# Kernel optimization log

Hardware: AMD Instinct MI355X
Metric: run time of the kernel (lower is better)

Reference implementation:

```python
import jax, jax.numpy as jnp
import numpy as np

B, S, D, H, T, R = 2, 2048, 768, 12, 64, 50
DH = D // H
EPS = 1e-12


def setup_inputs() -> dict:
    key = jax.random.key(0)
    ks = jax.random.split(key, 12)
    w = lambda k, shape: jax.random.normal(k, shape, jnp.float32) * 0.02
    inp = {
        "hidden_states": jax.random.normal(ks[0], (B, S, D), jnp.float32),
        "tag_emb": w(ks[1], (T, D)),
        "sa_wq": w(ks[2], (D, D)), "sa_bq": jnp.zeros((D,), jnp.float32),
        "sa_wk": w(ks[3], (D, D)), "sa_bk": jnp.zeros((D,), jnp.float32),
        "sa_wv": w(ks[4], (D, D)), "sa_bv": jnp.zeros((D,), jnp.float32),
        "sa_wo": w(ks[5], (D, D)), "sa_bo": jnp.zeros((D,), jnp.float32),
        "sa_ln_g": jnp.ones((D,), jnp.float32), "sa_ln_b": jnp.zeros((D,), jnp.float32),
        "ca_wq": w(ks[6], (D, D)), "ca_bq": jnp.zeros((D,), jnp.float32),
        "ca_wk": w(ks[7], (D, D)), "ca_bk": jnp.zeros((D,), jnp.float32),
        "ca_wv": w(ks[8], (D, D)), "ca_bv": jnp.zeros((D,), jnp.float32),
        "ca_wo": w(ks[9], (D, D)), "ca_bo": jnp.zeros((D,), jnp.float32),
        "ca_ln_g": jnp.ones((D,), jnp.float32), "ca_ln_b": jnp.zeros((D,), jnp.float32),
        "ff_w1": w(ks[10], (D, 3072)), "ff_b1": jnp.zeros((3072,), jnp.float32),
        "ff_w2": w(ks[11], (3072, D)), "ff_b2": jnp.zeros((D,), jnp.float32),
        "ff_ln_g": jnp.ones((D,), jnp.float32), "ff_ln_b": jnp.zeros((D,), jnp.float32),
    }
    return inp


def _layernorm(x, g, b):
    m = jnp.mean(x, axis=-1, keepdims=True)
    v = jnp.mean(jnp.square(x - m), axis=-1, keepdims=True)
    return (x - m) * jax.lax.rsqrt(v + EPS) * g + b


def _bert_attention(x, kv, mask, wq, bq, wk, bk, wv, bv, wo, bo, ln_g, ln_b):
    # BertSelfAttention: multi-head attn; mask (if any) is ADDED to scores (HF semantics).
    Bq, Sq = x.shape[0], x.shape[1]
    Sk = kv.shape[1]
    q = (x @ wq + bq).reshape(Bq, Sq, H, DH)
    k = (kv @ wk + bk).reshape(Bq, Sk, H, DH)
    v = (kv @ wv + bv).reshape(Bq, Sk, H, DH)
    scores = jnp.einsum("bqhd,bkhd->bhqk", q, k) / jnp.sqrt(jnp.float32(DH))
    if mask is not None:
        scores = scores + mask  # additive 0/1 band mask, as in the source
    probs = jax.nn.softmax(scores, axis=-1)
    ctx = jnp.einsum("bhqk,bkhd->bqhd", probs, v).reshape(Bq, Sq, D)
    # BertSelfOutput: dense + residual + LayerNorm
    return _layernorm(ctx @ wo + bo + x, ln_g, ln_b)


def reference(hidden_states, tag_emb,
              sa_wq, sa_bq, sa_wk, sa_bk, sa_wv, sa_bv, sa_wo, sa_bo, sa_ln_g, sa_ln_b,
              ca_wq, ca_bq, ca_wk, ca_bk, ca_wv, ca_bv, ca_wo, ca_bo, ca_ln_g, ca_ln_b,
              ff_w1, ff_b1, ff_w2, ff_b2, ff_ln_g, ff_ln_b):
    Sd = hidden_states.shape[1]
    # banded mask: tril(+R) * triu(-R) -> 1 inside window, 0 outside (added to scores)
    i = jnp.arange(Sd)
    band = (jnp.abs(i[:, None] - i[None, :]) <= R).astype(hidden_states.dtype)  # [S,S]
    attn_out = _bert_attention(hidden_states, hidden_states, band,
                               sa_wq, sa_bq, sa_wk, sa_bk, sa_wv, sa_bv,
                               sa_wo, sa_bo, sa_ln_g, sa_ln_b)
    tags = jnp.broadcast_to(tag_emb[None], (hidden_states.shape[0], T, D))
    attn_out = _bert_attention(attn_out, tags, None,
                               ca_wq, ca_bq, ca_wk, ca_bk, ca_wv, ca_bv,
                               ca_wo, ca_bo, ca_ln_g, ca_ln_b)
    # BertIntermediate + BertOutput (exact erf gelu as in HF)
    inter = jax.nn.gelu(attn_out @ ff_w1 + ff_b1, approximate=False)
    return _layernorm(inter @ ff_w2 + ff_b2 + attn_out, ff_ln_g, ff_ln_b)
```

## Files before the change

### kernel.cpp

```cpp
#include <hip/hip_runtime.h>
#include <cstdint>
#include <cstddef>


typedef __bf16 bf16;
typedef __bf16 bf16x8 __attribute__((ext_vector_type(8)));
typedef __bf16 bf16x4 __attribute__((ext_vector_type(4)));
typedef __bf16 bf16x2 __attribute__((ext_vector_type(2)));
typedef float  floatx4 __attribute__((ext_vector_type(4)));

__device__ __forceinline__ void glds16(const bf16* g, bf16* l) {
  __builtin_amdgcn_global_load_lds((const __attribute__((address_space(1))) void*)g,
                                   (__attribute__((address_space(3))) void*)l, 16, 0, 0);
}

__device__ __forceinline__ float fexp2(float x) {
  float r;
  asm("v_exp_f32 %0, %1" : "=v"(r) : "v"(x));
  return r;
}

__global__ __launch_bounds__(256) void k_prep_all(const float* __restrict__ sa_bq,
                                                  const float* __restrict__ sa_bk,
                                                  const float* __restrict__ sa_bv,
                                                  const float* __restrict__ ca_bk,
                                                  const float* __restrict__ ca_bv,
                                                  const float* __restrict__ tag,
                                                  const float* __restrict__ X,
                                                  float* __restrict__ bQKV,
                                                  float* __restrict__ bKV2,
                                                  bf16* __restrict__ tagp,
                                                  bf16* __restrict__ Xb) {
  int b = blockIdx.x, t = threadIdx.x;
  if (b < 9) {
    int i = b * 256 + t;
    int s = i / 768, j = i - s * 768;
    const float* p = s == 0 ? sa_bq : (s == 1 ? sa_bk : sa_bv);
    bQKV[i] = p[j];
  } else if (b < 15) {
    int i = (b - 9) * 256 + t;
    int s = i / 768, j = i - s * 768;
    bKV2[i] = s == 0 ? ca_bk[j] : ca_bv[j];
  } else if (b < 399) {
    int i = (b - 15) * 256 + t;
    if (i < 64 * 768) tagp[i] = (bf16)tag[i];
    else tagp[i] = (bf16)0.f;
  } else {
    int i = ((b - 399) * 256 + t) * 8;
    float4 a = *(const float4*)(X + i);
    float4 b4 = *(const float4*)(X + i + 4);
    bf16x8 o;
    o[0] = (bf16)a.x; o[1] = (bf16)a.y; o[2] = (bf16)a.z; o[3] = (bf16)a.w;
    o[4] = (bf16)b4.x; o[5] = (bf16)b4.y; o[6] = (bf16)b4.z; o[7] = (bf16)b4.w;
    *(bf16x8*)(Xb + i) = o;
  }
}

__device__ __forceinline__ void transpose_body(const float* __restrict__ W,
                                               bf16* __restrict__ Wt,
                                               int K, int N, int n0, int k0,
                                               bf16 (*tile)[72]) {
  int t = threadIdx.x;
  int r = t >> 2, cg = (t & 3) * 16;
  const float* src = W + (size_t)(k0 + r) * N + n0 + cg;
  float tmp[16];
  *(float4*)&tmp[0]  = *(const float4*)(src);
  *(float4*)&tmp[4]  = *(const float4*)(src + 4);
  *(float4*)&tmp[8]  = *(const float4*)(src + 8);
  *(float4*)&tmp[12] = *(const float4*)(src + 12);
#pragma unroll
  for (int i = 0; i < 16; ++i) tile[r][cg + i] = (bf16)tmp[i];
  __syncthreads();
  bf16* dst = Wt + (size_t)(n0 + r) * K + k0 + cg;
#pragma unroll
  for (int g = 0; g < 2; ++g) {
    bf16x8 pack;
#pragma unroll
    for (int i = 0; i < 8; ++i) pack[i] = tile[cg + g * 8 + i][r];
    *(bf16x8*)(dst + g * 8) = pack;
  }
}

__global__ __launch_bounds__(256) void k_transpose4(const float* __restrict__ W0,
                                                    const float* __restrict__ W1,
                                                    const float* __restrict__ W2w,
                                                    const float* __restrict__ W3,
                                                    bf16* __restrict__ Wt) {
  __shared__ bf16 tile[64][72];
  int z = blockIdx.z;
  const float* W = z == 0 ? W0 : (z == 1 ? W1 : (z == 2 ? W2w : W3));
  transpose_body(W, Wt + (size_t)z * 768 * 768, 768, 768,
                 blockIdx.x * 64, blockIdx.y * 64, tile);
}

__global__ __launch_bounds__(256) void k_transpose_ff(const float* __restrict__ ff_w1,
                                                      const float* __restrict__ ff_w2,
                                                      bf16* __restrict__ Wall,
                                                      bf16* __restrict__ W2) {
  __shared__ bf16 tile[64][72];
  if (blockIdx.z == 0)
    transpose_body(ff_w1, Wall, 768, 3072, blockIdx.x * 64, blockIdx.y * 64, tile);
  else
    transpose_body(ff_w2, W2, 3072, 768, blockIdx.y * 64, blockIdx.x * 64, tile);
}

template <int BM, int BN, int KS, bool CF32>
__device__ __forceinline__ void gemm_body(const bf16* __restrict__ Ab,
                                          const bf16* __restrict__ Bt,
                                          const float* __restrict__ bias,
                                          void* __restrict__ Co,
                                          int N, int K, int ld, int act,
                                          int m0, int n0,
                                          bf16* __restrict__ As,
                                          bf16* __restrict__ Bs) {
  constexpr int MT = BM / 32;
  constexpr int NT = BN / 32;
  constexpr int KSTEP = 32 * KS;
  int tid = threadIdx.x;
  int lane = tid & 63, wave = tid >> 6;
  int l16 = lane & 15, quad = lane >> 4;
  int wm = wave & 1, wn = wave >> 1;
  int arow = tid >> 2, acol = (tid & 3) * 8;
  int ldst = arow * 32 + acol;

  const bf16* Ap = Ab + (size_t)(m0 + arow) * ld + acol;
  const bf16* Bp = Bt + (size_t)(n0 + arow) * ld + acol;

  auto stage = [&](int k, int buf) {
    bf16* Asb = As + buf * (KS * BM * 32);
    bf16* Bsb = Bs + buf * (KS * BN * 32);
#pragma unroll
    for (int ks = 0; ks < KS; ++ks) {
      glds16(Bp + k + ks * 32, Bsb + ks * BN * 32 + ldst);
      if constexpr (BN == 128) glds16(Bp + (size_t)64 * ld + k + ks * 32, Bsb + ks * BN * 32 + ldst + 2048);
      glds16(Ap + k + ks * 32, Asb + ks * BM * 32 + ldst);
      if constexpr (BM == 128) glds16(Ap + (size_t)64 * ld + k + ks * 32, Asb + ks * BM * 32 + ldst + 2048);
    }
  };

  floatx4 acc[MT][NT];
#pragma unroll
  for (int i = 0; i < MT; ++i)
#pragma unroll
    for (int j = 0; j < NT; ++j) acc[i][j] = floatx4{0.f, 0.f, 0.f, 0.f};

  stage(0, 0);
  __syncthreads();

  int cur = 0;
  for (int k = 0; k < K; k += KSTEP) {
    if (k + KSTEP < K) stage(k + KSTEP, cur ^ 1);
    bf16* Asb = As + cur * (KS * BM * 32);
    bf16* Bsb = Bs + cur * (KS * BN * 32);
#pragma unroll
    for (int ks = 0; ks < KS; ++ks) {
      bf16x8 a_frag[MT], b_frag[NT];
#pragma unroll
      for (int mt = 0; mt < MT; ++mt)
        a_frag[mt] = *(const bf16x8*)(Asb + ks * BM * 32 + (wm * (BM / 2) + mt * 16 + l16) * 32 + quad * 8);
#pragma unroll
      for (int nt = 0; nt < NT; ++nt)
        b_frag[nt] = *(const bf16x8*)(Bsb + ks * BN * 32 + (wn * (BN / 2) + nt * 16 + l16) * 32 + quad * 8);
#pragma unroll
      for (int mt = 0; mt < MT; ++mt)
#pragma unroll
        for (int nt = 0; nt < NT; ++nt)
          acc[mt][nt] = __builtin_amdgcn_mfma_f32_16x16x32_bf16(a_frag[mt], b_frag[nt], acc[mt][nt], 0, 0, 0);
    }
    __syncthreads();
    cur ^= 1;
  }

#pragma unroll
  for (int nt = 0; nt < NT; ++nt) {
    int col = n0 + wn * (BN / 2) + nt * 16 + l16;
    float bv = bias ? bias[col] : 0.f;
#pragma unroll
    for (int mt = 0; mt < MT; ++mt) {
#pragma unroll
      for (int r = 0; r < 4; ++r) {
        int row = m0 + wm * (BM / 2) + mt * 16 + quad * 4 + r;
        float v = acc[mt][nt][r] + bv;
        if (act) v = 0.5f * v * (1.f + erff(v * 0.70710678118654752f));
        if constexpr (CF32) ((float*)Co)[(size_t)row * N + col] = v;
        else ((bf16*)Co)[(size_t)row * N + col] = (bf16)v;
      }
    }
  }
}

template <int BM, int BN, int KS, bool CF32>
__global__ __launch_bounds__(256) void k_gemm(const bf16* __restrict__ Ab,
                                              const bf16* __restrict__ Bt,
                                              const float* __restrict__ bias,
                                              void* __restrict__ Cv,
                                              void* __restrict__ Cv2,
                                              int N, int K, int ld, int act) {
  __shared__ bf16 As[2 * KS * BM * 32];
  __shared__ bf16 Bs[2 * KS * BN * 32];
  int z = blockIdx.z;
  gemm_body<BM, BN, KS, CF32>(Ab + z * K, Bt + z * K, z == 0 ? bias : nullptr,
                              z == 0 ? Cv : Cv2, N, K, ld, act,
                              blockIdx.x * BM, blockIdx.y * BN, As, Bs);
}

__global__ __launch_bounds__(256) void k_gemm_q2kv(const bf16* __restrict__ A0,
                                                   const bf16* __restrict__ B0,
                                                   const float* __restrict__ bias0,
                                                   bf16* __restrict__ C0,
                                                   const bf16* __restrict__ A1,
                                                   const bf16* __restrict__ B1,
                                                   const float* __restrict__ bias1,
                                                   bf16* __restrict__ C1) {
  __shared__ bf16 As[2 * 2 * 64 * 32];
  __shared__ bf16 Bs[2 * 2 * 64 * 32];
  if (blockIdx.z == 0) {
    gemm_body<64, 64, 2, false>(A0, B0, bias0, C0, 768, 768, 768, 0,
                                blockIdx.x * 64, blockIdx.y * 64, As, Bs);
  } else {
    if (blockIdx.y != 0 || blockIdx.x >= 48) return;
    gemm_body<64, 64, 2, false>(A1, B1, bias1, C1, 1536, 768, 768, 0,
                                (blockIdx.x & 1) * 64, (blockIdx.x >> 1) * 64, As, Bs);
  }
}

__global__ __launch_bounds__(256) void k_attn_mfma(const bf16* __restrict__ Q, int ldq,
                                                   const bf16* __restrict__ Kp,
                                                   const bf16* __restrict__ Vp, int ldkv,
                                                   bf16* __restrict__ O,
                                                   int S, int Skv,
                                                   long long kv_bstride, int bandR) {
  const int NH = 12;
  int qt = blockIdx.x, bh = blockIdx.y;
  int bb = bh / NH, h = bh % NH;
  const bf16* Qb = Q + (size_t)bb * S * ldq + h * 64;
  const bf16* Kb = Kp + (size_t)bb * kv_bstride + h * 64;
  const bf16* Vb = Vp + (size_t)bb * kv_bstride + h * 64;
  bf16* Ob = O + (size_t)bb * S * 768 + h * 64;

  __shared__ __align__(16) char smem[47104];
  float* Obuf = (float*)smem;
  float* l0_arr = (float*)(smem + 16896);

  int tid = threadIdx.x, wave = tid >> 6, lane = tid & 63;
  int quad = lane >> 4, l16 = lane & 15;
  int qh = wave & 1, kh = wave >> 1;
  bf16 (*Psw)[40] = (bf16(*)[40])(smem + 36864 + wave * 2560);

  const float C1 = 0.18033688f;
  const float C2 = 1.44269504f;

  int r = tid >> 2, cg = (tid & 3) * 16;
  int vk0 = 2 * (tid & 31);
  int vd0 = 8 * (tid >> 5);
  int vcol = (vk0 + 16 * (vd0 >> 4)) & 63;

  bf16x8 aq[2][2];
#pragma unroll
  for (int mt = 0; mt < 2; ++mt) {
    const bf16* qsrc = Qb + (size_t)(qt * 64 + qh * 32 + mt * 16 + l16) * ldq;
#pragma unroll
    for (int ks = 0; ks < 2; ++ks) {
      bf16x8 t = *(const bf16x8*)(qsrc + ks * 32 + quad * 8);
#pragma unroll
      for (int e = 0; e < 8; ++e) t[e] = (bf16)((float)t[e] * C1);
      aq[mt][ks] = t;
    }
  }

  bf16x8 ones;
#pragma unroll
  for (int e = 0; e < 8; ++e) ones[e] = (bf16)1.f;

  bf16x8 kr0, kr1, vr0, vr1;
  {
    const bf16* ksrc = Kb + (size_t)r * ldkv + cg;
    kr0 = *(const bf16x8*)ksrc;
    kr1 = *(const bf16x8*)(ksrc + 8);
    const bf16* vsrc = Vb + (size_t)vk0 * ldkv + vd0;
    vr0 = *(const bf16x8*)vsrc;
    vr1 = *(const bf16x8*)(vsrc + ldkv);
  }

  floatx4 accl[2];
  floatx4 acc[2][4];
#pragma unroll
  for (int mt = 0; mt < 2; ++mt) {
    accl[mt] = floatx4{0.f, 0.f, 0.f, 0.f};
#pragma unroll
    for (int j = 0; j < 4; ++j) acc[mt][j] = floatx4{0.f, 0.f, 0.f, 0.f};
  }

  int qi0 = qt * 64 + qh * 32 + quad * 4;

  for (int kc = 0; kc < Skv; kc += 64) {
    int cur = (kc >> 6) & 1;
    bf16 (*Ks)[72] = (bf16(*)[72])(smem + cur * 9216);
    bf16 (*Vt)[72] = (bf16(*)[72])(smem + 18432 + cur * 9216);
    *(bf16x8*)&Ks[r][cg] = kr0;
    *(bf16x8*)&Ks[r][cg + 8] = kr1;
#pragma unroll
    for (int e = 0; e < 8; ++e) {
      bf16x2 p; p[0] = vr0[e]; p[1] = vr1[e];
      *(bf16x2*)&Vt[vd0 + e][vcol] = p;
    }
    if (kc + 64 < Skv) {
      const bf16* ksrc = Kb + (size_t)(kc + 64 + r) * ldkv + cg;
      kr0 = *(const bf16x8*)ksrc;
      kr1 = *(const bf16x8*)(ksrc + 8);
      const bf16* vsrc = Vb + (size_t)(kc + 64 + vk0) * ldkv + vd0;
      vr0 = *(const bf16x8*)vsrc;
      vr1 = *(const bf16x8*)(vsrc + ldkv);
    }
    __syncthreads();

    floatx4 s[2][2];
    __builtin_amdgcn_s_setprio(1);
#pragma unroll
    for (int kt = 0; kt < 2; ++kt) {
      bf16x8 bk0 = *(const bf16x8*)&Ks[kh * 32 + kt * 16 + l16][quad * 8];
      bf16x8 bk1 = *(const bf16x8*)&Ks[kh * 32 + kt * 16 + l16][32 + quad * 8];
#pragma unroll
      for (int mt = 0; mt < 2; ++mt) {
        floatx4 c = {0.f, 0.f, 0.f, 0.f};
        c = __builtin_amdgcn_mfma_f32_16x16x32_bf16(aq[mt][0], bk0, c, 0, 0, 0);
        c = __builtin_amdgcn_mfma_f32_16x16x32_bf16(aq[mt][1], bk1, c, 0, 0, 0);
        s[mt][kt] = c;
      }
    }
    __builtin_amdgcn_s_setprio(0);

    bool masked = (bandR >= 0) && (kc <= qt * 64 + 63 + bandR) &&
                  (kc + 63 >= qt * 64 - bandR);
    if (masked) {
#pragma unroll
      for (int kt = 0; kt < 2; ++kt) {
        int kj = kc + kh * 32 + kt * 16 + l16;
        int colp = (kt * 16 + l16 + 8 * quad) & 31;
#pragma unroll
        for (int mt = 0; mt < 2; ++mt)
#pragma unroll
          for (int rr = 0; rr < 4; ++rr) {
            int d = qi0 + mt * 16 + rr - kj; if (d < 0) d = -d;
            float e = fexp2(s[mt][kt][rr] + (d <= bandR ? C2 : 0.f));
            Psw[mt * 16 + quad * 4 + rr][colp] = (bf16)e;
          }
      }
    } else {
#pragma unroll
      for (int kt = 0; kt < 2; ++kt) {
        int colp = (kt * 16 + l16 + 8 * quad) & 31;
#pragma unroll
        for (int mt = 0; mt < 2; ++mt)
#pragma unroll
          for (int rr = 0; rr < 4; ++rr) {
            float e = fexp2(s[mt][kt][rr]);
            Psw[mt * 16 + quad * 4 + rr][colp] = (bf16)e;
          }
      }
    }

    bf16x8 ap[2];
#pragma unroll
    for (int mt = 0; mt < 2; ++mt)
      ap[mt] = *(const bf16x8*)&Psw[mt * 16 + l16][8 * ((quad + (l16 >> 2)) & 3)];
    __builtin_amdgcn_s_setprio(1);
#pragma unroll
    for (int mt = 0; mt < 2; ++mt)
      accl[mt] = __builtin_amdgcn_mfma_f32_16x16x32_bf16(ap[mt], ones, accl[mt], 0, 0, 0);
#pragma unroll
    for (int nt = 0; nt < 4; ++nt) {
      bf16x8 bv = *(const bf16x8*)&Vt[nt * 16 + l16][(kh * 32 + quad * 8 + 16 * nt) & 63];
#pragma unroll
      for (int mt = 0; mt < 2; ++mt)
        acc[mt][nt] = __builtin_amdgcn_mfma_f32_16x16x32_bf16(ap[mt], bv, acc[mt][nt], 0, 0, 0);
    }
    __builtin_amdgcn_s_setprio(0);
  }

  __syncthreads();
  if (kh == 0) {
#pragma unroll
    for (int mt = 0; mt < 2; ++mt)
#pragma unroll
      for (int nt = 0; nt < 4; ++nt)
#pragma unroll
        for (int rr = 0; rr < 4; ++rr)
          Obuf[(qh * 32 + mt * 16 + quad * 4 + rr) * 66 + nt * 16 + l16] = acc[mt][nt][rr];
    if (l16 == 0) {
#pragma unroll
      for (int mt = 0; mt < 2; ++mt)
#pragma unroll
        for (int rr = 0; rr < 4; ++rr)
          l0_arr[qh * 32 + mt * 16 + quad * 4 + rr] = accl[mt][rr];
    }
  }
  __syncthreads();
  if (kh == 1) {
#pragma unroll
    for (int mt = 0; mt < 2; ++mt)
#pragma unroll
      for (int rr = 0; rr < 4; ++rr) {
        int ql = qh * 32 + mt * 16 + quad * 4 + rr;
        float lt = accl[mt][rr] + l0_arr[ql];
        int qrow = qt * 64 + ql;
#pragma unroll
        for (int nt = 0; nt < 4; ++nt) {
          float o = (acc[mt][nt][rr] + Obuf[ql * 66 + nt * 16 + l16]) / lt;
          Ob[(size_t)qrow * 768 + nt * 16 + l16] = (bf16)o;
        }
      }
  }
}

template <typename TY, typename TR, typename TO>
__global__ __launch_bounds__(256) void k_add_ln(const TY* __restrict__ Y,
                                                const TR* __restrict__ X,
                                                const float* __restrict__ Y2,
                                                const float* __restrict__ g,
                                                const float* __restrict__ b,
                                                TO* __restrict__ out) {
  int wave = threadIdx.x >> 6, lane = threadIdx.x & 63;
  int row = blockIdx.x * 4 + wave;
  const TY* y = Y + (size_t)row * 768;
  const TR* x = X + (size_t)row * 768;
  float v[12];
  float s = 0.f, s2 = 0.f;
#pragma unroll
  for (int c = 0; c < 3; ++c) {
    int idx = c * 256 + lane * 4;
    float yv[4], xv[4];
    if constexpr (__is_same(TY, float)) {
      float4 t = *(const float4*)(y + idx);
      yv[0] = t.x; yv[1] = t.y; yv[2] = t.z; yv[3] = t.w;
    } else {
      bf16x4 t = *(const bf16x4*)(y + idx);
#pragma unroll
      for (int i = 0; i < 4; ++i) yv[i] = (float)t[i];
    }
    if constexpr (__is_same(TR, float)) {
      float4 t = *(const float4*)(x + idx);
      xv[0] = t.x; xv[1] = t.y; xv[2] = t.z; xv[3] = t.w;
    } else {
      bf16x4 t = *(const bf16x4*)(x + idx);
#pragma unroll
      for (int i = 0; i < 4; ++i) xv[i] = (float)t[i];
    }
    if (Y2 != nullptr) {
      float4 t2 = *(const float4*)(Y2 + (size_t)row * 768 + idx);
      xv[0] += t2.x; xv[1] += t2.y; xv[2] += t2.z; xv[3] += t2.w;
    }
#pragma unroll
    for (int i = 0; i < 4; ++i) {
      float t = yv[i] + xv[i];
      v[c * 4 + i] = t; s += t; s2 += t * t;
    }
  }
#pragma unroll
  for (int off = 32; off > 0; off >>= 1) { s += __shfl_xor(s, off); s2 += __shfl_xor(s2, off); }
  float mean = s * (1.f / 768.f);
  float var = fmaxf(s2 * (1.f / 768.f) - mean * mean, 0.f);
  float inv = rsqrtf(var + 1e-12f);
  TO* o = out + (size_t)row * 768;
#pragma unroll
  for (int c = 0; c < 3; ++c) {
    int idx = c * 256 + lane * 4;
    float4 gv = *(const float4*)(g + idx);
    float4 bv = *(const float4*)(b + idx);
    float r0 = (v[c * 4 + 0] - mean) * inv * gv.x + bv.x;
    float r1 = (v[c * 4 + 1] - mean) * inv * gv.y + bv.y;
    float r2 = (v[c * 4 + 2] - mean) * inv * gv.z + bv.z;
    float r3 = (v[c * 4 + 3] - mean) * inv * gv.w + bv.w;
    if constexpr (__is_same(TO, float)) {
      float4 ov = {r0, r1, r2, r3};
      *(float4*)(o + idx) = ov;
    } else {
      bf16x4 ov;
      ov[0] = (bf16)r0; ov[1] = (bf16)r1; ov[2] = (bf16)r2; ov[3] = (bf16)r3;
      *(bf16x4*)(o + idx) = ov;
    }
  }
}

extern "C" void kernel_launch(void* const* d_in, const int* in_sizes, int n_in,
                              void* d_out, int out_size, void* d_ws, size_t ws_size,
                              hipStream_t stream) {
  (void)in_sizes; (void)n_in; (void)out_size; (void)ws_size;
  const float* X     = (const float*)d_in[0];
  const float* tag   = (const float*)d_in[1];
  const float* sa_wq = (const float*)d_in[2];
  const float* sa_bq = (const float*)d_in[3];
  const float* sa_wk = (const float*)d_in[4];
  const float* sa_bk = (const float*)d_in[5];
  const float* sa_wv = (const float*)d_in[6];
  const float* sa_bv = (const float*)d_in[7];
  const float* sa_wo = (const float*)d_in[8];
  const float* sa_bo = (const float*)d_in[9];
  const float* sa_lg = (const float*)d_in[10];
  const float* sa_lb = (const float*)d_in[11];
  const float* ca_wq = (const float*)d_in[12];
  const float* ca_bq = (const float*)d_in[13];
  const float* ca_wk = (const float*)d_in[14];
  const float* ca_bk = (const float*)d_in[15];
  const float* ca_wv = (const float*)d_in[16];
  const float* ca_bv = (const float*)d_in[17];
  const float* ca_wo = (const float*)d_in[18];
  const float* ca_bo = (const float*)d_in[19];
  const float* ca_lg = (const float*)d_in[20];
  const float* ca_lb = (const float*)d_in[21];
  const float* ff_w1 = (const float*)d_in[22];
  const float* ff_b1 = (const float*)d_in[23];
  const float* ff_w2 = (const float*)d_in[24];
  const float* ff_b2 = (const float*)d_in[25];
  const float* ff_lg = (const float*)d_in[26];
  const float* ff_lb = (const float*)d_in[27];

  float* outf = (float*)d_out;
  bf16* outb = (bf16*)d_out;
  const size_t SLOT = (size_t)4096 * 768;

  bf16* BIG   = (bf16*)d_ws;
  bf16* slotA = BIG + (size_t)4096 * 2304;
  bf16* Wall  = slotA + SLOT;
  bf16* W2    = Wall + (size_t)3072 * 768;
  bf16* tagp  = W2;
  bf16* k2v2  = W2 + (size_t)128 * 768;
  float* bQKV = (float*)(W2 + (size_t)128 * 768 + (size_t)128 * 1536);
  float* bKV2 = bQKV + 2304;
  float* P1   = (float*)(BIG + 2 * SLOT);
  bf16*  Xb   = outb + SLOT;

  dim3 blk(256);

  k_prep_all<<<dim3(1935), blk, 0, stream>>>(sa_bq, sa_bk, sa_bv, ca_bk, ca_bv, tag, X,
                                             bQKV, bKV2, tagp, Xb);

  k_transpose4<<<dim3(12, 12, 4), blk, 0, stream>>>(sa_wq, sa_wk, sa_wv, sa_wo, Wall);
  k_gemm<128, 64, 2, false><<<dim3(32, 36), blk, 0, stream>>>(Xb, Wall, bQKV, BIG, nullptr,
                                                              2304, 768, 768, 0);
  k_attn_mfma<<<dim3(32, 24), blk, 0, stream>>>(BIG, 2304, BIG + 768, BIG + 1536, 2304,
                                                outb, 2048, 2048, (long long)2048 * 2304, 50);
  k_gemm<64, 64, 2, false><<<dim3(64, 12), blk, 0, stream>>>(outb, Wall + (size_t)2304 * 768,
                                                             sa_bo, slotA, nullptr,
                                                             768, 768, 768, 0);
  k_transpose4<<<dim3(12, 12, 4), blk, 0, stream>>>(ca_wq, ca_wk, ca_wv, ca_wo, Wall);
  k_add_ln<bf16, float, bf16><<<dim3(1024), blk, 0, stream>>>(slotA, X, nullptr, sa_lg, sa_lb, slotA);

  k_gemm_q2kv<<<dim3(64, 12, 2), blk, 0, stream>>>(slotA, Wall, ca_bq, BIG,
                                                   tagp, Wall + (size_t)768 * 768, bKV2, k2v2);
  k_attn_mfma<<<dim3(32, 24), blk, 0, stream>>>(BIG, 768, k2v2, k2v2 + 768, 1536,
                                                outb, 2048, 64, 0, -1);
  k_gemm<64, 64, 2, false><<<dim3(64, 12), blk, 0, stream>>>(outb, Wall + (size_t)2304 * 768,
                                                             ca_bo, BIG + SLOT, nullptr,
                                                             768, 768, 768, 0);
  k_add_ln<bf16, bf16, bf16><<<dim3(1024), blk, 0, stream>>>(BIG + SLOT, slotA, nullptr,
                                                             ca_lg, ca_lb, slotA);

  k_transpose_ff<<<dim3(48, 12, 2), blk, 0, stream>>>(ff_w1, ff_w2, Wall, W2);
  for (int mc = 0; mc < 2; ++mc) {
    const bf16* a2 = slotA + (size_t)mc * 2048 * 768;
    float* yo = outf + (size_t)mc * 2048 * 768;
    k_gemm<128, 64, 2, false><<<dim3(16, 48), blk, 0, stream>>>(a2, Wall, ff_b1, BIG, nullptr,
                                                                3072, 768, 768, 1);
    k_gemm<64, 64, 2, true><<<dim3(32, 12, 2), blk, 0, stream>>>(BIG, W2, ff_b2, yo, P1,
                                                                 768, 1536, 3072, 0);
    k_add_ln<float, bf16, float><<<dim3(512), blk, 0, stream>>>(yo, a2, P1, ff_lg, ff_lb, yo);
  }
}
```

Measured before the change: 383.5 us.

## Stage attention K/V via direct global-to-LDS loads and transpose-read V

Replaces the register-staged K/V loads and the manual V transpose scatter into LDS with global_load_lds async copies into swizzled LDS buffers. V is now read with ds_read_b64_tr_b16, which transposes in hardware, so the per-element bf16x2 scatter stores are gone. This frees VGPRs and shrinks LDS use. It relies on intricate swizzle index math, and the explicit lgkmcnt wait plus sched_barrier may serialise the LDS reads against the MFMAs.

```diff
diff --git a/kernel.cpp b/kernel.cpp
--- a/kernel.cpp
+++ b/kernel.cpp
@@ -8,6 +8,7 @@
 typedef __bf16 bf16x4 __attribute__((ext_vector_type(4)));
 typedef __bf16 bf16x2 __attribute__((ext_vector_type(2)));
 typedef float  floatx4 __attribute__((ext_vector_type(4)));
+typedef unsigned uint32x2 __attribute__((ext_vector_type(2)));
 
 __device__ __forceinline__ void glds16(const bf16* g, bf16* l) {
   __builtin_amdgcn_global_load_lds((const __attribute__((address_space(1))) void*)g,
@@ -238,22 +239,35 @@
   const bf16* Vb = Vp + (size_t)bb * kv_bstride + h * 64;
   bf16* Ob = O + (size_t)bb * S * 768 + h * 64;
 
-  __shared__ __align__(16) char smem[47104];
+  __shared__ __align__(16) char smem[43008];
   float* Obuf = (float*)smem;
   float* l0_arr = (float*)(smem + 16896);
 
   int tid = threadIdx.x, wave = tid >> 6, lane = tid & 63;
   int quad = lane >> 4, l16 = lane & 15;
   int qh = wave & 1, kh = wave >> 1;
-  bf16 (*Psw)[40] = (bf16(*)[40])(smem + 36864 + wave * 2560);
+  bf16 (*Psw)[40] = (bf16(*)[40])(smem + 32768 + wave * 2560);
 
   const float C1 = 0.18033688f;
   const float C2 = 1.44269504f;
 
-  int r = tid >> 2, cg = (tid & 3) * 16;
-  int vk0 = 2 * (tid & 31);
-  int vd0 = 8 * (tid >> 5);
-  int vcol = (vk0 + 16 * (vd0 >> 4)) & 63;
+  int L0 = wave * 1024 + lane * 16;
+  int L1 = L0 + 4096;
+  int krow0 = L0 >> 7, kcol0 = ((L0 & 127) ^ ((krow0 & 7) << 4)) >> 1;
+  int krow1 = L1 >> 7, kcol1 = ((L1 & 127) ^ ((krow1 & 7) << 4)) >> 1;
+  int vk0s, vd0s, vk1s, vd1s;
+  {
+    int slot = L0 >> 7;
+    int kb = ((slot >> 2) & 1) * 8 + (slot & 3) * 2 + ((slot >> 3) & 1);
+    vk0s = kb * 4 + ((L0 >> 5) & 3);
+    vd0s = (slot >> 4) * 16 + ((L0 >> 1) & 8);
+  }
+  {
+    int slot = L1 >> 7;
+    int kb = ((slot >> 2) & 1) * 8 + (slot & 3) * 2 + ((slot >> 3) & 1);
+    vk1s = kb * 4 + ((L1 >> 5) & 3);
+    vd1s = (slot >> 4) * 16 + ((L1 >> 1) & 8);
+  }
 
   bf16x8 aq[2][2];
 #pragma unroll
@@ -272,15 +286,17 @@
 #pragma unroll
   for (int e = 0; e < 8; ++e) ones[e] = (bf16)1.f;
 
-  bf16x8 kr0, kr1, vr0, vr1;
-  {
-    const bf16* ksrc = Kb + (size_t)r * ldkv + cg;
-    kr0 = *(const bf16x8*)ksrc;
-    kr1 = *(const bf16x8*)(ksrc + 8);
-    const bf16* vsrc = Vb + (size_t)vk0 * ldkv + vd0;
-    vr0 = *(const bf16x8*)vsrc;
-    vr1 = *(const bf16x8*)(vsrc + ldkv);
-  }
+  unsigned vbase = (unsigned)(uintptr_t)(__attribute__((address_space(3))) char*)(smem + 16384);
+  unsigned vlane = (unsigned)(((kh * 4 + quad) * 64 + l16) * 2);
+
+  auto stage = [&](int kcb, int buf) {
+    char* kd = smem + buf * 8192;
+    char* vd = smem + 16384 + buf * 8192;
+    glds16(Kb + (size_t)(kcb + krow0) * ldkv + kcol0, (bf16*)(kd + L0));
+    glds16(Kb + (size_t)(kcb + krow1) * ldkv + kcol1, (bf16*)(kd + L1));
+    glds16(Vb + (size_t)(kcb + vk0s) * ldkv + vd0s, (bf16*)(vd + L0));
+    glds16(Vb + (size_t)(kcb + vk1s) * ldkv + vd1s, (bf16*)(vd + L1));
+  };
 
   floatx4 accl[2];
   floatx4 acc[2][4];
@@ -293,33 +309,21 @@
 
   int qi0 = qt * 64 + qh * 32 + quad * 4;
 
+  stage(0, 0);
   for (int kc = 0; kc < Skv; kc += 64) {
     int cur = (kc >> 6) & 1;
-    bf16 (*Ks)[72] = (bf16(*)[72])(smem + cur * 9216);
-    bf16 (*Vt)[72] = (bf16(*)[72])(smem + 18432 + cur * 9216);
-    *(bf16x8*)&Ks[r][cg] = kr0;
-    *(bf16x8*)&Ks[r][cg + 8] = kr1;
-#pragma unroll
-    for (int e = 0; e < 8; ++e) {
-      bf16x2 p; p[0] = vr0[e]; p[1] = vr1[e];
-      *(bf16x2*)&Vt[vd0 + e][vcol] = p;
-    }
-    if (kc + 64 < Skv) {
-      const bf16* ksrc = Kb + (size_t)(kc + 64 + r) * ldkv + cg;
-      kr0 = *(const bf16x8*)ksrc;
-      kr1 = *(const bf16x8*)(ksrc + 8);
-      const bf16* vsrc = Vb + (size_t)(kc + 64 + vk0) * ldkv + vd0;
-      vr0 = *(const bf16x8*)vsrc;
-      vr1 = *(const bf16x8*)(vsrc + ldkv);
-    }
     __syncthreads();
-
+    if (kc + 64 < Skv) stage(kc + 64, cur ^ 1);
+
+    const char* kbase = smem + cur * 8192;
     floatx4 s[2][2];
     __builtin_amdgcn_s_setprio(1);
 #pragma unroll
     for (int kt = 0; kt < 2; ++kt) {
-      bf16x8 bk0 = *(const bf16x8*)&Ks[kh * 32 + kt * 16 + l16][quad * 8];
-      bf16x8 bk1 = *(const bf16x8*)&Ks[kh * 32 + kt * 16 + l16][32 + quad * 8];
+      int rowA = kh * 32 + kt * 16 + l16;
+      int sw = (rowA & 7) << 4;
+      bf16x8 bk0 = *(const bf16x8*)(kbase + rowA * 128 + ((quad * 16) ^ sw));
+      bf16x8 bk1 = *(const bf16x8*)(kbase + rowA * 128 + ((quad * 16 + 64) ^ sw));
 #pragma unroll
       for (int mt = 0; mt < 2; ++mt) {
         floatx4 c = {0.f, 0.f, 0.f, 0.f};
@@ -364,13 +368,33 @@
 #pragma unroll
     for (int mt = 0; mt < 2; ++mt)
       ap[mt] = *(const bf16x8*)&Psw[mt * 16 + l16][8 * ((quad + (l16 >> 2)) & 3)];
+
+    unsigned va = vbase + (unsigned)(cur * 8192) + vlane;
+    uint32x2 u0, u1, u2, u3, u4, u5, u6, u7;
+    asm volatile("ds_read_b64_tr_b16 %0, %1 offset:0"    : "=v"(u0) : "v"(va));
+    asm volatile("ds_read_b64_tr_b16 %0, %1 offset:1024" : "=v"(u1) : "v"(va));
+    asm volatile("ds_read_b64_tr_b16 %0, %1 offset:2048" : "=v"(u2) : "v"(va));
+    asm volatile("ds_read_b64_tr_b16 %0, %1 offset:3072" : "=v"(u3) : "v"(va));
+    asm volatile("ds_read_b64_tr_b16 %0, %1 offset:4096" : "=v"(u4) : "v"(va));
+    asm volatile("ds_read_b64_tr_b16 %0, %1 offset:5120" : "=v"(u5) : "v"(va));
+    asm volatile("ds_read_b64_tr_b16 %0, %1 offset:6144" : "=v"(u6) : "v"(va));
+    asm volatile("ds_read_b64_tr_b16 %0, %1 offset:7168" : "=v"(u7) : "v"(va));
+    asm volatile("s_waitcnt lgkmcnt(0)" ::: "memory");
+    __builtin_amdgcn_sched_barrier(0);
+
+    bf16x4 vlo[4], vhi[4];
+    vlo[0] = __builtin_bit_cast(bf16x4, u0); vhi[0] = __builtin_bit_cast(bf16x4, u1);
+    vlo[1] = __builtin_bit_cast(bf16x4, u2); vhi[1] = __builtin_bit_cast(bf16x4, u3);
+    vlo[2] = __builtin_bit_cast(bf16x4, u4); vhi[2] = __builtin_bit_cast(bf16x4, u5);
+    vlo[3] = __builtin_bit_cast(bf16x4, u6); vhi[3] = __builtin_bit_cast(bf16x4, u7);
+
     __builtin_amdgcn_s_setprio(1);
 #pragma unroll
     for (int mt = 0; mt < 2; ++mt)
       accl[mt] = __builtin_amdgcn_mfma_f32_16x16x32_bf16(ap[mt], ones, accl[mt], 0, 0, 0);
 #pragma unroll
     for (int nt = 0; nt < 4; ++nt) {
-      bf16x8 bv = *(const bf16x8*)&Vt[nt * 16 + l16][(kh * 32 + quad * 8 + 16 * nt) & 63];
+      bf16x8 bv = __builtin_shufflevector(vlo[nt], vhi[nt], 0, 1, 2, 3, 4, 5, 6, 7);
 #pragma unroll
       for (int mt = 0; mt < 2; ++mt)
         acc[mt][nt] = __builtin_amdgcn_mfma_f32_16x16x32_bf16(ap[mt], bv, acc[mt][nt], 0, 0, 0);
```

Measured after the change: 380.0 us. No clear change (-0.9%).
